# Kernel tuning notes

Measured on AMD Instinct MI355X. Metric: run time of the kernel, lower is better.

## Reference

```python
import jax, jax.numpy as jnp
import numpy as np

B, D, NF, L, G = 8192, 4096, 16, 32, 64  # batch, input_dim, num_factors, latent_per_factor, num groups
K = D // G  # group size (contiguous equal-size partition of columns)


def setup_inputs() -> dict:
    key = jax.random.key(0)
    k0, k1, k2, k3 = jax.random.split(key, 4)
    x = jax.random.normal(k0, (B, D), dtype=jnp.float32)
    # encoder: Linear(D,128) -> ReLU -> Linear(128, NF*L)
    W1 = jax.random.normal(k1, (D, 128), dtype=jnp.float32) * 0.02
    b1 = jnp.zeros((128,), dtype=jnp.float32)
    W2 = jax.random.normal(k2, (128, NF * L), dtype=jnp.float32) * 0.02
    b2 = jnp.zeros((NF * L,), dtype=jnp.float32)
    # k_matrix decoders: one [K, L] matrix per group, stacked -> [G, K, L]
    decoders = jax.random.normal(k3, (G, K, L), dtype=jnp.float32)
    return {"x": x, "W1": W1, "b1": b1, "W2": W2, "b2": b2, "decoders": decoders}


def reference(x, W1, b1, W2, b2, decoders):
    # encoder
    z = jax.nn.relu(x @ W1 + b1) @ W2 + b2                 # [B, NF*L]
    # reconstructions[:, group_g] = sum_j z_j @ D_g^T  ==  (sum_j z_j) @ D_g^T
    z_sum = z.reshape(x.shape[0], NF, L).sum(axis=1)        # [B, L]
    recon = jnp.einsum('bl,gkl->bgk', z_sum, decoders)      # [B, G, K]
    recon = recon.reshape(x.shape[0], G * K)                # [B, D] (contiguous groups)
    return (z, recon)
```

## Files before the change

kernel.cpp:

```cpp
#include <hip/hip_runtime.h>
#include <hip/hip_bf16.h>

#define BATCH 8192
#define DIN   4096
#define H1    128
#define NLAT  512
#define LAT   32
#define BM    16
#define BKW   64
#define WSTEPS 8
#define ABUF  1024
#define PP    130

typedef short bf16x8 __attribute__((ext_vector_type(8)));
typedef short bf16x4 __attribute__((ext_vector_type(4)));
typedef float f32x4  __attribute__((ext_vector_type(4)));

static __device__ __forceinline__ unsigned short f2bf(float f) {
  union { float f; unsigned u; } v; v.f = f;
  return (unsigned short)((v.u + 0x7FFFu + ((v.u >> 16) & 1u)) >> 16);
}
static __device__ __forceinline__ float bf2f(unsigned short u) {
  union { unsigned u; float f; } v; v.u = ((unsigned)u) << 16; return v.f;
}
static __device__ __forceinline__ void cvtw8(unsigned short* p, f32x4 a, f32x4 b) {
  union { bf16x8 v; unsigned short u[8]; } o;
#pragma unroll
  for (int j = 0; j < 4; j++) { o.u[j] = f2bf(a[j]); o.u[4 + j] = f2bf(b[j]); }
  *(bf16x8*)p = o.v;
}

__global__ void prep_all(const float* __restrict__ W1, const float* __restrict__ W2,
                         const float* __restrict__ dec,
                         unsigned short* __restrict__ W1B,
                         unsigned short* __restrict__ W2B,
                         float* __restrict__ decT) {
  int b = blockIdx.x;
  int t = threadIdx.x;
  if (b < 256) {
    int gi = (b << 2) + (t >> 6);
    int lane = t & 63;
    int kb = ((gi >> 3) << 5) + ((lane >> 4) << 3);
    int c = ((gi & 7) << 4) + (lane & 15);
    union { bf16x8 v; unsigned short u[8]; } o;
#pragma unroll
    for (int j = 0; j < 8; j++) o.u[j] = f2bf(W1[(size_t)(kb + j) * H1 + c]);
    *(bf16x8*)(W1B + (((size_t)gi << 6) + lane) * 8) = o.v;
  } else if (b < 288) {
    int gi = ((b - 256) << 2) + (t >> 6);
    int lane = t & 63;
    int kb = ((gi >> 5) << 5) + ((lane >> 4) << 3);
    int c = ((gi & 31) << 4) + (lane & 15);
    union { bf16x8 v; unsigned short u[8]; } o;
#pragma unroll
    for (int j = 0; j < 8; j++) o.u[j] = f2bf(W2[(size_t)(kb + j) * NLAT + c]);
    *(bf16x8*)(W2B + (((size_t)gi << 6) + lane) * 8) = o.v;
  } else {
    __shared__ float tbuf[32][33];
    int d0 = (b - 288) * 32;
    int tx = t & 31, ty = t >> 5;
#pragma unroll
    for (int i = 0; i < 32; i += 8)
      tbuf[ty + i][tx] = dec[(size_t)(d0 + ty + i) * LAT + tx];
    __syncthreads();
#pragma unroll
    for (int i = 0; i < 32; i += 8)
      decT[(size_t)(ty + i) * DIN + (d0 + tx)] = tbuf[tx][ty + i];
  }
}

__global__ __launch_bounds__(512, 4) void enc_kernel(
    const float* __restrict__ x, const unsigned short* __restrict__ W1B,
    const unsigned short* __restrict__ W2B,
    const float* __restrict__ b1, const float* __restrict__ b2,
    float* __restrict__ zout, float* __restrict__ zsumg) {
  __shared__ __align__(16) unsigned char smem[70144];
  unsigned short* Apriv = (unsigned short*)smem;
  unsigned short* pacc  = (unsigned short*)(smem + 32768);
  unsigned short* hs    = (unsigned short*)(smem + 66048);
  float* zsp            = (float*)smem;

  const int t = threadIdx.x;
  const int rbase = blockIdx.x << 4;
  const int w = t >> 6, lane = t & 63;
  const int g = lane >> 4, fr = lane & 15;

  const int srow = lane >> 2, sq = lane & 3;
  const float* xp = x + (size_t)(rbase + srow) * DIN + (w << 9) + (sq << 4);
  unsigned short* abase = Apriv + (w << 11);
  const int wg0 = ((sq << 1) ^ (srow & 7)) << 3;
  const int wg1 = (((sq << 1) | 1) ^ (srow & 7)) << 3;

  f32x4 acc[8];
#pragma unroll
  for (int i = 0; i < 8; i++) acc[i] = (f32x4){0.f, 0.f, 0.f, 0.f};

  f32x4 pA0, pA1, pA2, pA3, pB0, pB1, pB2, pB3;
#define LOADPF(P, S) do {                              \
    const float* np_ = xp + (S) * BKW;                 \
    P##0 = *(const f32x4*)np_;                         \
    P##1 = *(const f32x4*)(np_ + 4);                   \
    P##2 = *(const f32x4*)(np_ + 8);                   \
    P##3 = *(const f32x4*)(np_ + 12);                  \
  } while (0)

  LOADPF(pA, 0);
  LOADPF(pB, 1);
  {
    unsigned short* wr = abase + srow * 64;
    cvtw8(wr + wg0, pA0, pA1);
    cvtw8(wr + wg1, pA2, pA3);
  }

#define STEP(S, PAR, PFW, PFL) do {                                          \
    if ((S) + 2 < WSTEPS) LOADPF(PFL, (S) + 2);                              \
    const unsigned short* ab_ = abase + (PAR) * ABUF;                        \
    const int kbase_ = (w << 4) + ((S) << 1);                                \
    _Pragma("unroll")                                                        \
    for (int k32l = 0; k32l < 2; ++k32l) {                                   \
      bf16x8 a_ = *(const bf16x8*)(ab_ + fr * 64 +                           \
                    ((((k32l << 2) + g) ^ (fr & 7)) << 3));                  \
      const unsigned short* bp_ =                                            \
          W1B + (((size_t)(kbase_ + k32l) << 3) << 9) + (lane << 3);         \
      _Pragma("unroll")                                                      \
      for (int cf = 0; cf < 8; ++cf) {                                       \
        bf16x8 bv_ = *(const bf16x8*)(bp_ + ((size_t)cf << 9));              \
        acc[cf] = __builtin_amdgcn_mfma_f32_16x16x32_bf16(a_, bv_, acc[cf], 0, 0, 0); \
      }                                                                      \
    }                                                                        \
    if ((S) + 1 < WSTEPS) {                                                  \
      unsigned short* wr_ = abase + ((PAR) ^ 1) * ABUF + srow * 64;          \
      cvtw8(wr_ + wg0, PFW##0, PFW##1);                                      \
      cvtw8(wr_ + wg1, PFW##2, PFW##3);                                      \
    }                                                                        \
  } while (0)

  for (int s2 = 0; s2 < WSTEPS; s2 += 2) {
    STEP(s2 + 0, 0, pB, pA);
    STEP(s2 + 1, 1, pA, pB);
  }
#undef STEP
#undef LOADPF

#pragma unroll
  for (int cf = 0; cf < 8; ++cf)
#pragma unroll
    for (int j = 0; j < 4; ++j)
      pacc[(w * BM + (g << 2) + j) * PP + (cf << 4) + fr] = f2bf(acc[cf][j]);
  __syncthreads();

  {
    const int r = t >> 5, c4 = (t & 31) << 2;
    float s0 = b1[c4], s1 = b1[c4 + 1], s2 = b1[c4 + 2], s3 = b1[c4 + 3];
#pragma unroll
    for (int wv = 0; wv < 8; ++wv) {
      union { bf16x4 v; unsigned short u[4]; } p;
      p.v = *(const bf16x4*)&pacc[(wv * BM + r) * PP + c4];
      s0 += bf2f(p.u[0]); s1 += bf2f(p.u[1]); s2 += bf2f(p.u[2]); s3 += bf2f(p.u[3]);
    }
    union { bf16x4 v; unsigned short u[4]; } o;
    o.u[0] = f2bf(fmaxf(s0, 0.f)); o.u[1] = f2bf(fmaxf(s1, 0.f));
    o.u[2] = f2bf(fmaxf(s2, 0.f)); o.u[3] = f2bf(fmaxf(s3, 0.f));
    const int gi = c4 >> 3;
    *(bf16x4*)(hs + (r << 7) + ((gi ^ (r & 15)) << 3) + (c4 & 7)) = o.v;
  }
  __syncthreads();

  f32x4 acc2[4];
#pragma unroll
  for (int i = 0; i < 4; i++) acc2[i] = (f32x4){0.f, 0.f, 0.f, 0.f};
#pragma unroll
  for (int k32 = 0; k32 < 4; ++k32) {
    bf16x8 a0 = *(const bf16x8*)(hs + (fr << 7) +
                  ((((k32 << 2) + g) ^ (fr & 15)) << 3));
#pragma unroll
    for (int cc = 0; cc < 4; ++cc) {
      bf16x8 bv = *(const bf16x8*)(W2B +
          (((size_t)((k32 << 5) + (w << 2) + cc)) << 9) + (lane << 3));
      acc2[cc] = __builtin_amdgcn_mfma_f32_16x16x32_bf16(a0, bv, acc2[cc], 0, 0, 0);
    }
  }
  {
    f32x4 zv[4];
#pragma unroll
    for (int cc = 0; cc < 4; ++cc) {
      const float b2v = b2[(w << 6) + (cc << 4) + fr];
#pragma unroll
      for (int j = 0; j < 4; j++) zv[cc][j] = acc2[cc][j] + b2v;
    }
    const int row0 = g << 2;
#pragma unroll
    for (int j = 0; j < 4; j++) {
#pragma unroll
      for (int cc = 0; cc < 4; ++cc)
        zout[(size_t)(rbase + row0 + j) * NLAT + (w << 6) + (cc << 4) + fr] = zv[cc][j];
      zsp[(w * BM + row0 + j) * 33 + fr]      = zv[0][j] + zv[2][j];
      zsp[(w * BM + row0 + j) * 33 + 16 + fr] = zv[1][j] + zv[3][j];
    }
  }
  __syncthreads();
  {
    const int r = t >> 5, l = t & 31;
    float s = 0.f;
#pragma unroll
    for (int wv = 0; wv < 8; ++wv) s += zsp[(wv * BM + r) * 33 + l];
    zsumg[(size_t)(rbase + r) * LAT + l] = s;
  }
}

__global__ __launch_bounds__(256) void recon_kernel(
    const float* __restrict__ zsumg, const float* __restrict__ decT,
    float* __restrict__ rout) {
  __shared__ float zs[32][32];
  int t = threadIdx.x;
  int rbase = (blockIdx.x >> 4) << 5;
  int dcol0 = (blockIdx.x & 15) << 8;
  {
    int r = t >> 3, c4 = (t & 7) << 2;
    *(f32x4*)&zs[r][c4] = *(const f32x4*)(zsumg + (size_t)(rbase + r) * LAT + c4);
  }
  __syncthreads();
  int wq = t >> 6, lane = t & 63;
  int r0 = wq << 3;
  int dcol = dcol0 + (lane << 2);
  f32x4 acc[8];
#pragma unroll
  for (int r = 0; r < 8; r++) acc[r] = (f32x4){0.f, 0.f, 0.f, 0.f};
#pragma unroll 4
  for (int l = 0; l < 32; l++) {
    f32x4 dv = *(const f32x4*)(decT + (size_t)l * DIN + dcol);
#pragma unroll
    for (int r = 0; r < 8; r++) {
      float zv = zs[r0 + r][l];
#pragma unroll
      for (int j = 0; j < 4; j++) acc[r][j] += zv * dv[j];
    }
  }
#pragma unroll
  for (int r = 0; r < 8; r++)
    *(f32x4*)(rout + (size_t)(rbase + r0 + r) * DIN + dcol) = acc[r];
}

extern "C" void kernel_launch(void* const* d_in, const int* in_sizes, int n_in,
                              void* d_out, int out_size, void* d_ws, size_t ws_size,
                              hipStream_t stream) {
  const float* x   = (const float*)d_in[0];
  const float* W1  = (const float*)d_in[1];
  const float* b1  = (const float*)d_in[2];
  const float* W2  = (const float*)d_in[3];
  const float* b2  = (const float*)d_in[4];
  const float* dec = (const float*)d_in[5];
  float* zout = (float*)d_out;
  float* rout = zout + (size_t)BATCH * NLAT;

  char* ws = (char*)d_ws;
  unsigned short* W1B = (unsigned short*)ws;
  unsigned short* W2B = (unsigned short*)(ws + (1u << 20));
  float* decT  = (float*)(ws + (1u << 20) + (1u << 17));
  float* zsumg = (float*)(ws + (1u << 20) + (1u << 17) + (1u << 19));

  prep_all<<<dim3(416), 256, 0, stream>>>(W1, W2, dec, W1B, W2B, decT);
  enc_kernel<<<dim3(BATCH / BM), 512, 0, stream>>>(x, W1B, W2B, b1, b2, zout, zsumg);
  recon_kernel<<<dim3(4096), 256, 0, stream>>>(zsumg, decT, rout);
}
```

Measured before the change: 92.09 us.

## Load x directly into MFMA fragments, dropping LDS staging and prefetch pipeline

Replaces the double-buffered LDS staging of x tiles, with swizzled writes and register prefetch, by direct global loads of each lane's 8-element fragment. Each fragment is converted to bf16 in registers and fed straight to MFMA, so shared memory only holds the reduction buffers. This cuts LDS traffic and shared memory size. In exchange, global loads become less coalesced (32-byte chunks per lane across 16 rows) and explicit prefetch is lost; launch_bounds min blocks drops from 4 to 2.

```diff
diff --git a/kernel.cpp b/kernel.cpp
--- a/kernel.cpp
+++ b/kernel.cpp
@@ -7,9 +7,6 @@
 #define NLAT  512
 #define LAT   32
 #define BM    16
-#define BKW   64
-#define WSTEPS 8
-#define ABUF  1024
 #define PP    130
 
 typedef short bf16x8 __attribute__((ext_vector_type(8)));
@@ -22,12 +19,6 @@
 }
 static __device__ __forceinline__ float bf2f(unsigned short u) {
   union { unsigned u; float f; } v; v.u = ((unsigned)u) << 16; return v.f;
-}
-static __device__ __forceinline__ void cvtw8(unsigned short* p, f32x4 a, f32x4 b) {
-  union { bf16x8 v; unsigned short u[8]; } o;
-#pragma unroll
-  for (int j = 0; j < 4; j++) { o.u[j] = f2bf(a[j]); o.u[4 + j] = f2bf(b[j]); }
-  *(bf16x8*)p = o.v;
 }
 
 __global__ void prep_all(const float* __restrict__ W1, const float* __restrict__ W2,
@@ -69,78 +60,40 @@
   }
 }
 
-__global__ __launch_bounds__(512, 4) void enc_kernel(
+__global__ __launch_bounds__(512, 2) void enc_kernel(
     const float* __restrict__ x, const unsigned short* __restrict__ W1B,
     const unsigned short* __restrict__ W2B,
     const float* __restrict__ b1, const float* __restrict__ b2,
     float* __restrict__ zout, float* __restrict__ zsumg) {
-  __shared__ __align__(16) unsigned char smem[70144];
-  unsigned short* Apriv = (unsigned short*)smem;
-  unsigned short* pacc  = (unsigned short*)(smem + 32768);
-  unsigned short* hs    = (unsigned short*)(smem + 66048);
-  float* zsp            = (float*)smem;
+  __shared__ unsigned short pacc[8 * BM * PP];
+  __shared__ unsigned short hs[16 * 128];
+  __shared__ float zsp[8 * BM * 33];
 
   const int t = threadIdx.x;
   const int rbase = blockIdx.x << 4;
   const int w = t >> 6, lane = t & 63;
   const int g = lane >> 4, fr = lane & 15;
 
-  const int srow = lane >> 2, sq = lane & 3;
-  const float* xp = x + (size_t)(rbase + srow) * DIN + (w << 9) + (sq << 4);
-  unsigned short* abase = Apriv + (w << 11);
-  const int wg0 = ((sq << 1) ^ (srow & 7)) << 3;
-  const int wg1 = (((sq << 1) | 1) ^ (srow & 7)) << 3;
-
   f32x4 acc[8];
 #pragma unroll
   for (int i = 0; i < 8; i++) acc[i] = (f32x4){0.f, 0.f, 0.f, 0.f};
 
-  f32x4 pA0, pA1, pA2, pA3, pB0, pB1, pB2, pB3;
-#define LOADPF(P, S) do {                              \
-    const float* np_ = xp + (S) * BKW;                 \
-    P##0 = *(const f32x4*)np_;                         \
-    P##1 = *(const f32x4*)(np_ + 4);                   \
-    P##2 = *(const f32x4*)(np_ + 8);                   \
-    P##3 = *(const f32x4*)(np_ + 12);                  \
-  } while (0)
-
-  LOADPF(pA, 0);
-  LOADPF(pB, 1);
-  {
-    unsigned short* wr = abase + srow * 64;
-    cvtw8(wr + wg0, pA0, pA1);
-    cvtw8(wr + wg1, pA2, pA3);
-  }
-
-#define STEP(S, PAR, PFW, PFL) do {                                          \
-    if ((S) + 2 < WSTEPS) LOADPF(PFL, (S) + 2);                              \
-    const unsigned short* ab_ = abase + (PAR) * ABUF;                        \
-    const int kbase_ = (w << 4) + ((S) << 1);                                \
-    _Pragma("unroll")                                                        \
-    for (int k32l = 0; k32l < 2; ++k32l) {                                   \
-      bf16x8 a_ = *(const bf16x8*)(ab_ + fr * 64 +                           \
-                    ((((k32l << 2) + g) ^ (fr & 7)) << 3));                  \
-      const unsigned short* bp_ =                                            \
-          W1B + (((size_t)(kbase_ + k32l) << 3) << 9) + (lane << 3);         \
-      _Pragma("unroll")                                                      \
-      for (int cf = 0; cf < 8; ++cf) {                                       \
-        bf16x8 bv_ = *(const bf16x8*)(bp_ + ((size_t)cf << 9));              \
-        acc[cf] = __builtin_amdgcn_mfma_f32_16x16x32_bf16(a_, bv_, acc[cf], 0, 0, 0); \
-      }                                                                      \
-    }                                                                        \
-    if ((S) + 1 < WSTEPS) {                                                  \
-      unsigned short* wr_ = abase + ((PAR) ^ 1) * ABUF + srow * 64;          \
-      cvtw8(wr_ + wg0, PFW##0, PFW##1);                                      \
-      cvtw8(wr_ + wg1, PFW##2, PFW##3);                                      \
-    }                                                                        \
-  } while (0)
-
-  for (int s2 = 0; s2 < WSTEPS; s2 += 2) {
-    STEP(s2 + 0, 0, pB, pA);
-    STEP(s2 + 1, 1, pA, pB);
-  }
-#undef STEP
-#undef LOADPF
+  const float* arow = x + (size_t)(rbase + fr) * DIN + (w << 9) + (g << 3);
+#pragma unroll 4
+  for (int c = 0; c < 16; ++c) {
+    f32x4 a0 = *(const f32x4*)(arow + (c << 5));
+    f32x4 a1 = *(const f32x4*)(arow + (c << 5) + 4);
+    union { bf16x8 v; unsigned short u[8]; } af;
+#pragma unroll
+    for (int j = 0; j < 4; j++) { af.u[j] = f2bf(a0[j]); af.u[4 + j] = f2bf(a1[j]); }
+    const unsigned short* bp =
+        W1B + (((size_t)((w << 4) + c) << 3) << 9) + (lane << 3);
+#pragma unroll
+    for (int cf = 0; cf < 8; ++cf) {
+      bf16x8 bv = *(const bf16x8*)(bp + ((size_t)cf << 9));
+      acc[cf] = __builtin_amdgcn_mfma_f32_16x16x32_bf16(af.v, bv, acc[cf], 0, 0, 0);
+    }
+  }
 
 #pragma unroll
   for (int cf = 0; cf < 8; ++cf)
```

New measurement: 96.30 us. 1.05x slower.
